# Optimization experiments

Hardware: AMD Instinct MI355X
Metric: run time of the kernel (lower is better)

Reference implementation:

```python
import jax, jax.numpy as jnp
import numpy as np

N, E, B, PG = 20000, 320000, 20, 1000  # nodes, edges, graphs, nodes-per-graph
H, L, NB, EI = 256, 6, 16, 8           # hidden, layers, node_base_dim, edge_in_dim
LN_EPS = 1e-5


def setup_inputs() -> dict:
    key = jax.random.key(0)
    ks = jax.random.split(key, 32)
    w = lambda i, s: (jax.random.normal(ks[i], s, jnp.float32) * 0.05)
    inp = {
        "x": jax.random.normal(ks[0], (N, NB), jnp.float32),
        "edge_attr": jax.random.normal(ks[1], (E, EI), jnp.float32),
        "c": jax.random.normal(ks[2], (B, PG), jnp.float32),
        "edge_index": jax.random.randint(ks[3], (2, E), 0, N),
        "node_gid": jnp.arange(N) // PG,   # batch.batch
        "node_lid": jnp.arange(N) % PG,    # node local index
        # edge_mlp: Linear(EI,H), ReLU, Linear(H,H)
        "ew1": w(4, (EI, H)), "eb1": jnp.zeros((H,), jnp.float32),
        "ew2": w(5, (H, H)),  "eb2": jnp.zeros((H,), jnp.float32),
        # input_proj: Linear(NB+1, H), SiLU
        "in_w": w(6, (NB + 1, H)), "in_b": jnp.zeros((H,), jnp.float32),
        # per-layer GINEConv edge lin (edge_dim -> in_channels)
        "lin_w": w(7, (L, H, H)), "lin_b": jnp.zeros((L, H), jnp.float32),
        # per-layer conv MLP: Linear(H,H), SiLU, Linear(H,H)
        "cw1": w(8, (L, H, H)), "cb1": jnp.zeros((L, H), jnp.float32),
        "cw2": w(9, (L, H, H)), "cb2": jnp.zeros((L, H), jnp.float32),
        # per-layer LayerNorm
        "ln_g": jnp.ones((L, H), jnp.float32), "ln_b": jnp.zeros((L, H), jnp.float32),
        # pool_attn: Linear(H,H), Tanh, Linear(H,1)
        "pa_w1": w(10, (H, H)), "pa_b1": jnp.zeros((H,), jnp.float32),
        "pa_w2": w(11, (H, 1)), "pa_b2": jnp.zeros((1,), jnp.float32),
        # head: Linear(H,H), SiLU, Linear(H,1)
        "hw1": w(12, (H, H)), "hb1": jnp.zeros((H,), jnp.float32),
        "hw2": w(13, (H, 1)), "hb2": jnp.zeros((1,), jnp.float32),
    }
    return inp


def _layer_norm(z, g, b):
    m = jnp.mean(z, axis=-1, keepdims=True)
    v = jnp.mean(jnp.square(z - m), axis=-1, keepdims=True)
    return (z - m) * jax.lax.rsqrt(v + LN_EPS) * g + b


def reference(x, edge_attr, c, edge_index, node_gid, node_lid,
              ew1, eb1, ew2, eb2, in_w, in_b,
              lin_w, lin_b, cw1, cb1, cw2, cb2, ln_g, ln_b,
              pa_w1, pa_b1, pa_w2, pa_b2, hw1, hb1, hw2, hb2):
    silu = jax.nn.silu
    # c_scalar: per-node coefficient
    c_scalar = c[node_gid, node_lid][:, None]                       # [N,1]
    xin = jnp.concatenate([x, c_scalar], axis=-1)                   # [N,NB+1]
    e = jax.nn.relu(edge_attr @ ew1 + eb1) @ ew2 + eb2              # [E,H]
    h = silu(xin @ in_w + in_b)                                     # [N,H]
    src, dst = edge_index[0], edge_index[1]
    for l in range(L):
        msg = jax.nn.relu(h[src] + (e @ lin_w[l] + lin_b[l]))       # [E,H]
        agg = jnp.zeros_like(h).at[dst].add(msg)                    # scatter-add
        z = h + agg                                                 # (1+eps)*x_i + agg, eps=0
        h_new = silu(z @ cw1[l] + cb1[l]) @ cw2[l] + cb2[l]
        h_new = _layer_norm(h_new, ln_g[l], ln_b[l])
        h = h + silu(h_new)
    # attention pooling: global softmax over nodes, renormalized per graph
    scores = jnp.tanh(h @ pa_w1 + pa_b1) @ pa_w2 + pa_b2            # [N,1]
    attn = jax.nn.softmax(scores, axis=0)                           # [N,1]
    seg_sum = jax.ops.segment_sum(attn[:, 0], node_gid, num_segments=B)  # [B]
    attn_n = attn[:, 0] / (seg_sum[node_gid] + 1e-8)                # [N]
    pooled = jax.ops.segment_sum(h * attn_n[:, None], node_gid, num_segments=B)  # [B,H]
    q = (silu(pooled @ hw1 + hb1) @ hw2 + hb2)[:, 0]                # [B]
    return q
```

## Files before the change

### kernel.cpp

```cpp
#include <hip/hip_runtime.h>
#include <hip/hip_bf16.h>
#include <cstdint>


#define NN 20000
#define EE 320000
#define BBG 20
#define PGN 1000
#define HH 256
#define LL 6

typedef short bf16x8 __attribute__((ext_vector_type(8)));
typedef float f32x4 __attribute__((ext_vector_type(4)));

__device__ __forceinline__ void async16(const void* g, void* l) {
  __builtin_amdgcn_global_load_lds(
      (const __attribute__((address_space(1))) unsigned int*)(uintptr_t)g,
      (__attribute__((address_space(3))) unsigned int*)(uintptr_t)l, 16, 0, 0);
}

__device__ __forceinline__ float siluf(float x) { return x / (1.f + __expf(-x)); }

__device__ __forceinline__ unsigned int f2bu(float x) {
  __hip_bfloat16 h = __float2bfloat16(x);
  return (unsigned int)*(unsigned short*)&h;
}

__device__ __forceinline__ float b2f(unsigned short u) {
  unsigned int v = ((unsigned int)u) << 16;
  return *(float*)&v;
}

enum { EPI_SILU = 1, EPI_PLAIN = 2, EPI_TANH = 3 };

template <int EPI>
__global__ void __launch_bounds__(256, 2) gemm256(
    const __hip_bfloat16* __restrict__ A, const __hip_bfloat16* __restrict__ Wt,
    const float* __restrict__ bias, int M, float* __restrict__ outf,
    __hip_bfloat16* __restrict__ outb) {
  __shared__ __align__(16) __hip_bfloat16 sA[128 * 32];
  __shared__ __align__(16) __hip_bfloat16 sB[128 * 32];

  const int t = threadIdx.x;
  const int wave = t >> 6, lane = t & 63;
  const int row0 = blockIdx.x * 128;
  const int col0 = blockIdx.y * 128;

  const int wrow = (wave >> 1) * 64;
  const int wcol = (wave & 1) * 64;
  const int fr = lane & 15, q = lane >> 4;

  f32x4 zero = {0.f, 0.f, 0.f, 0.f};
  f32x4 acc[4][4];
#pragma unroll
  for (int i = 0; i < 4; i++)
#pragma unroll
    for (int j = 0; j < 4; j++) acc[i][j] = zero;

  const int c1 = t, c2 = t + 256;
  const int lr1 = c1 >> 2, lr2 = c2 >> 2;
  const int q1 = (c1 & 3) ^ ((lr1 >> 1) & 3);
  const int q2 = (c2 & 3) ^ ((lr2 >> 1) & 3);
  int rA1 = row0 + lr1; if (rA1 >= M) rA1 = M - 1;
  int rA2 = row0 + lr2; if (rA2 >= M) rA2 = M - 1;
  const int rB1 = col0 + lr1, rB2 = col0 + lr2;

  for (int k0 = 0; k0 < 256; k0 += 32) {
    async16((const char*)(A + (size_t)rA1 * HH + k0) + q1 * 16,
            (char*)sA + wave * 1024);
    async16((const char*)(A + (size_t)rA2 * HH + k0) + q2 * 16,
            (char*)sA + 4096 + wave * 1024);
    async16((const char*)(Wt + (size_t)rB1 * HH + k0) + q1 * 16,
            (char*)sB + wave * 1024);
    async16((const char*)(Wt + (size_t)rB2 * HH + k0) + q2 * 16,
            (char*)sB + 4096 + wave * 1024);
    __syncthreads();
    bf16x8 af[4], bfr[4];
#pragma unroll
    for (int i = 0; i < 4; i++) {
      const int row = wrow + i * 16 + fr;
      af[i] = *(const bf16x8*)&sA[row * 32 + ((q ^ ((row >> 1) & 3))) * 8];
    }
#pragma unroll
    for (int j = 0; j < 4; j++) {
      const int row = wcol + j * 16 + fr;
      bfr[j] = *(const bf16x8*)&sB[row * 32 + ((q ^ ((row >> 1) & 3))) * 8];
    }
#pragma unroll
    for (int i = 0; i < 4; i++)
#pragma unroll
      for (int j = 0; j < 4; j++)
        acc[i][j] = __builtin_amdgcn_mfma_f32_16x16x32_bf16(af[i], bfr[j],
                                                            acc[i][j], 0, 0, 0);
    __syncthreads();
  }

#pragma unroll
  for (int j = 0; j < 4; j++) {
    const int col = col0 + wcol + j * 16 + fr;
    const float bs = bias[col];
#pragma unroll
    for (int i = 0; i < 4; i++) {
      const int lr0 = wrow + i * 16 + q * 4;
#pragma unroll
      for (int r = 0; r < 4; r++) {
        const int grow = row0 + lr0 + r;
        float v = acc[i][j][r] + bs;
        if (grow < M) {
          if (EPI == EPI_SILU) {
            outb[(size_t)grow * HH + col] = __float2bfloat16(siluf(v));
          } else if (EPI == EPI_PLAIN) {
            outf[(size_t)grow * HH + col] = v;
          } else {
            outb[(size_t)grow * HH + col] = __float2bfloat16(tanhf(v));
          }
        }
      }
    }
  }
}

__global__ void __launch_bounds__(256, 2) mlp_ln(
    const float* __restrict__ z, const __hip_bfloat16* __restrict__ W1t,
    const float* __restrict__ b1, const __hip_bfloat16* __restrict__ W2t,
    const float* __restrict__ b2, const float* __restrict__ g,
    const float* __restrict__ bbv, float* __restrict__ h,
    float* __restrict__ yzf, __hip_bfloat16* __restrict__ hb) {
  __shared__ __align__(16) char smem[20480 + 64 * 264 * 2];
  __hip_bfloat16* sA = (__hip_bfloat16*)smem;
  __hip_bfloat16* sB = (__hip_bfloat16*)(smem + 4096);
  unsigned short* sT = (unsigned short*)(smem + 20480);

  const int t = threadIdx.x;
  const int wave = t >> 6, lane = t & 63;
  const int row0 = blockIdx.x * 64;
  const int fr = lane & 15, q = lane >> 4;
  const int wr = wave * 16;

  const int lrA = t >> 2;
  const int qA = (t & 3) ^ ((lrA >> 1) & 3);
  int rA = row0 + lrA; if (rA >= NN) rA = NN - 1;
  int qB[4], rB[4];
#pragma unroll
  for (int p = 0; p < 4; p++) {
    const int c = t + p * 256;
    const int lr = c >> 2;
    qB[p] = (c & 3) ^ ((lr >> 1) & 3);
    rB[p] = lr;
  }

  f32x4 zero = {0.f, 0.f, 0.f, 0.f};
  f32x4 acc[16];
#pragma unroll
  for (int j = 0; j < 16; j++) acc[j] = zero;

  for (int k0 = 0; k0 < 256; k0 += 32) {
    {
      const float* s1 = z + (size_t)rA * HH + k0 + qA * 8;
      float4 a0 = *(const float4*)s1;
      float4 a1 = *(const float4*)(s1 + 4);
      uint4 u;
      u.x = f2bu(a0.x) | (f2bu(a0.y) << 16);
      u.y = f2bu(a0.z) | (f2bu(a0.w) << 16);
      u.z = f2bu(a1.x) | (f2bu(a1.y) << 16);
      u.w = f2bu(a1.z) | (f2bu(a1.w) << 16);
      *(uint4*)((char*)sA + t * 16) = u;
    }
#pragma unroll
    for (int p = 0; p < 4; p++)
      async16((const char*)(W1t + (size_t)rB[p] * HH + k0) + qB[p] * 16,
              (char*)sB + p * 4096 + wave * 1024);
    __syncthreads();
    bf16x8 af;
    {
      const int row = wr + fr;
      af = *(const bf16x8*)&sA[row * 32 + ((q ^ ((row >> 1) & 3))) * 8];
    }
#pragma unroll
    for (int j = 0; j < 16; j++) {
      const int row = j * 16 + fr;
      bf16x8 bfr = *(const bf16x8*)&sB[row * 32 + ((q ^ ((row >> 1) & 3))) * 8];
      acc[j] = __builtin_amdgcn_mfma_f32_16x16x32_bf16(af, bfr, acc[j], 0, 0, 0);
    }
    __syncthreads();
  }
#pragma unroll
  for (int j = 0; j < 16; j++) {
    const int col = j * 16 + fr;
    const float bs = b1[col];
    const int r0 = wr + q * 4;
#pragma unroll
    for (int r = 0; r < 4; r++)
      sT[(r0 + r) * 264 + col] =
          (unsigned short)f2bu(siluf(acc[j][r] + bs));
  }
#pragma unroll
  for (int j = 0; j < 16; j++) acc[j] = zero;

  for (int k0 = 0; k0 < 256; k0 += 32) {
#pragma unroll
    for (int p = 0; p < 4; p++)
      async16((const char*)(W2t + (size_t)rB[p] * HH + k0) + qB[p] * 16,
              (char*)sB + p * 4096 + wave * 1024);
    __syncthreads();
    bf16x8 af = *(const bf16x8*)&sT[(wr + fr) * 264 + k0 + q * 8];
#pragma unroll
    for (int j = 0; j < 16; j++) {
      const int row = j * 16 + fr;
      bf16x8 bfr = *(const bf16x8*)&sB[row * 32 + ((q ^ ((row >> 1) & 3))) * 8];
      acc[j] = __builtin_amdgcn_mfma_f32_16x16x32_bf16(af, bfr, acc[j], 0, 0, 0);
    }
    __syncthreads();
  }
#pragma unroll
  for (int j = 0; j < 16; j++) {
    const int col = j * 16 + fr;
    const float bs = b2[col];
    const int r0 = wr + q * 4;
#pragma unroll
    for (int r = 0; r < 4; r++)
      sT[(r0 + r) * 264 + col] = (unsigned short)f2bu(acc[j][r] + bs);
  }
  __syncthreads();

  for (int rr = 0; rr < 16; rr++) {
    const int r = wr + rr;
    const int grow = row0 + r;
    if (grow >= NN) break;
    float v[4];
    float s = 0.f;
#pragma unroll
    for (int i = 0; i < 4; i++) {
      v[i] = b2f(sT[r * 264 + lane + i * 64]);
      s += v[i];
    }
#pragma unroll
    for (int o = 32; o; o >>= 1) s += __shfl_xor(s, o);
    const float mean = s * (1.f / 256.f);
    float var = 0.f;
#pragma unroll
    for (int i = 0; i < 4; i++) { float d = v[i] - mean; var += d * d; }
#pragma unroll
    for (int o = 32; o; o >>= 1) var += __shfl_xor(var, o);
    const float rs = rsqrtf(var * (1.f / 256.f) + 1e-5f);
#pragma unroll
    for (int i = 0; i < 4; i++) {
      const int c = lane + i * 64;
      float ln = (v[i] - mean) * rs * g[c] + bbv[c];
      float si = siluf(ln);
      size_t idx = (size_t)grow * HH + c;
      float nh = h[idx] + si;
      h[idx] = nh;
      yzf[idx] = nh;
      hb[idx] = __float2bfloat16(nh);
    }
  }
}

__global__ void __launch_bounds__(256, 4) edge_fused(
    const __hip_bfloat16* __restrict__ te, const __hip_bfloat16* __restrict__ Wt,
    const float* __restrict__ bias, const __hip_bfloat16* __restrict__ hbv,
    const int* __restrict__ srcp, const int* __restrict__ dstp,
    float* __restrict__ z) {
  __shared__ __align__(16) char smem[32768];
  __shared__ int sSrc[128], sDst[128];
  __hip_bfloat16* sA = (__hip_bfloat16*)smem;
  __hip_bfloat16* sB = (__hip_bfloat16*)(smem + 16384);
  unsigned short* sRed = (unsigned short*)smem;

  const int t = threadIdx.x;
  const int wave = t >> 6, lane = t & 63;
  const int row0 = blockIdx.y * 128;
  const int col0 = blockIdx.x * 128;

  if (t < 128) { sSrc[t] = srcp[row0 + t]; sDst[t] = dstp[row0 + t]; }
  __syncthreads();

  const int wrow = (wave >> 1) * 64;
  const int fr = lane & 15, q = lane >> 4;
  const int rc = lane, rb = wave;

  f32x4 zero = {0.f, 0.f, 0.f, 0.f};
  f32x4 acc[4][4];
#pragma unroll
  for (int i = 0; i < 4; i++)
#pragma unroll
    for (int j = 0; j < 4; j++) acc[i][j] = zero;

  const int c1 = t, c2 = t + 256;
  const int lr1 = c1 >> 2, lr2 = c2 >> 2;
  const int q1 = (c1 & 3) ^ ((lr1 >> 1) & 3);
  const int q2 = (c2 & 3) ^ ((lr2 >> 1) & 3);
  const int rA1 = row0 + lr1, rA2 = row0 + lr2;
  const int rB1 = col0 + lr1, rB2 = col0 + lr2;

#pragma unroll
  for (int it = 0; it < 4; it++) {
    const int ka = it * 64, kb = ka + 32;
    async16((const char*)(te + (size_t)rA1 * HH + ka) + q1 * 16,
            (char*)sA + wave * 1024);
    async16((const char*)(te + (size_t)rA2 * HH + ka) + q2 * 16,
            (char*)sA + 4096 + wave * 1024);
    async16((const char*)(te + (size_t)rA1 * HH + kb) + q1 * 16,
            (char*)sA + 8192 + wave * 1024);
    async16((const char*)(te + (size_t)rA2 * HH + kb) + q2 * 16,
            (char*)sA + 12288 + wave * 1024);
    async16((const char*)(Wt + (size_t)rB1 * HH + ka) + q1 * 16,
            (char*)sB + wave * 1024);
    async16((const char*)(Wt + (size_t)rB2 * HH + ka) + q2 * 16,
            (char*)sB + 4096 + wave * 1024);
    async16((const char*)(Wt + (size_t)rB1 * HH + kb) + q1 * 16,
            (char*)sB + 8192 + wave * 1024);
    async16((const char*)(Wt + (size_t)rB2 * HH + kb) + q2 * 16,
            (char*)sB + 12288 + wave * 1024);
    __syncthreads();
#pragma unroll
    for (int half = 0; half < 2; half++) {
      const __hip_bfloat16* pA = sA + half * 4096;
      const __hip_bfloat16* pB = sB + half * 4096;
      bf16x8 af[4], bfr[4];
#pragma unroll
      for (int i = 0; i < 4; i++) {
        const int row = wrow + i * 16 + fr;
        af[i] = *(const bf16x8*)&pA[row * 32 + ((q ^ ((row >> 1) & 3))) * 8];
      }
#pragma unroll
      for (int j = 0; j < 4; j++) {
        const int row = (wave & 1) * 64 + j * 16 + fr;
        bfr[j] = *(const bf16x8*)&pB[row * 32 + ((q ^ ((row >> 1) & 3))) * 8];
      }
#pragma unroll
      for (int i = 0; i < 4; i++)
#pragma unroll
        for (int j = 0; j < 4; j++)
          acc[i][j] = __builtin_amdgcn_mfma_f32_16x16x32_bf16(af[i], bfr[j],
                                                              acc[i][j], 0, 0, 0);
    }
    __syncthreads();
  }

#pragma unroll
  for (int hf = 0; hf < 2; hf++) {
    if ((wave & 1) == hf) {
#pragma unroll
      for (int j = 0; j < 4; j++) {
        const int cl = j * 16 + fr;
        const float bs = bias[col0 + hf * 64 + cl];
#pragma unroll
        for (int i = 0; i < 4; i++) {
          const int r0 = wrow + i * 16 + q * 4;
          f32x4 v = acc[i][j];
          unsigned int p0 = f2bu(v[0] + bs) | (f2bu(v[1] + bs) << 16);
          unsigned int p1 = f2bu(v[2] + bs) | (f2bu(v[3] + bs) << 16);
          *(unsigned int*)&sRed[cl * 130 + r0] = p0;
          *(unsigned int*)&sRed[cl * 130 + r0 + 2] = p1;
        }
      }
    }
    __syncthreads();
    const int gcol = col0 + hf * 64 + rc;
    float a = 0.f;
    int cur = sDst[rb * 32];
    for (int ch = 0; ch < 4; ch++) {
      float hv8[8];
#pragma unroll
      for (int u = 0; u < 8; u++)
        hv8[u] = __bfloat162float(
            hbv[(size_t)sSrc[rb * 32 + ch * 8 + u] * HH + gcol]);
#pragma unroll
      for (int u = 0; u < 8; u++) {
        const int row = rb * 32 + ch * 8 + u;
        const int d = sDst[row];
        if (d != cur) {
          unsafeAtomicAdd(&z[(size_t)cur * HH + gcol], a);
          a = 0.f;
          cur = d;
        }
        float m = b2f(sRed[rc * 130 + row]) + hv8[u];
        a += m > 0.f ? m : 0.f;
      }
    }
    unsafeAtomicAdd(&z[(size_t)cur * HH + gcol], a);
    __syncthreads();
  }
}

__global__ void __launch_bounds__(256) hist_k(const int* __restrict__ edst,
                                              int* __restrict__ cnt) {
  const int e = blockIdx.x * 256 + threadIdx.x;
  if (e < EE) atomicAdd(&cnt[edst[e]], 1);
}

__global__ void __launch_bounds__(256) scan_k(const int* __restrict__ cnt,
                                              int* __restrict__ rowptr) {
  __shared__ int wsum[4];
  __shared__ int carry;
  const int t = threadIdx.x, wave = t >> 6, lane = t & 63;
  if (t == 0) carry = 0;
  __syncthreads();
  for (int base = 0; base < NN; base += 256) {
    const int idx = base + t;
    int v = (idx < NN) ? cnt[idx] : 0;
    int inc = v;
#pragma unroll
    for (int o = 1; o < 64; o <<= 1) {
      int u = __shfl_up(inc, o);
      if (lane >= o) inc += u;
    }
    if (lane == 63) wsum[wave] = inc;
    __syncthreads();
    int woff = 0;
    for (int w2 = 0; w2 < wave; w2++) woff += wsum[w2];
    if (idx < NN) rowptr[idx] = carry + woff + inc - v;
    const int total = wsum[0] + wsum[1] + wsum[2] + wsum[3];
    __syncthreads();
    if (t == 0) carry += total;
    __syncthreads();
  }
  if (t == 0) rowptr[NN] = carry;
}

__global__ void __launch_bounds__(256) scatter_k(
    const int* __restrict__ esrc, const int* __restrict__ edst,
    int* __restrict__ cursor, int* __restrict__ posof,
    int* __restrict__ srcp, int* __restrict__ dstp) {
  const int e = blockIdx.x * 256 + threadIdx.x;
  if (e < EE) {
    const int d = edst[e];
    const int pos = atomicAdd(&cursor[d], 1);
    posof[e] = pos;
    srcp[pos] = esrc[e];
    dstp[pos] = d;
  }
}

__global__ void __launch_bounds__(256) edge_hidden(
    const float* __restrict__ ea, const float* __restrict__ ew1,
    const float* __restrict__ eb1, const int* __restrict__ posof,
    __hip_bfloat16* __restrict__ tout) {
  __shared__ float w[8 * 256];
  __shared__ float b[256];
  __shared__ float sea[16 * 8];
  __shared__ int spos[16];
  const int t = threadIdx.x;
  for (int i = t; i < 8 * 256; i += 256) w[i] = ew1[i];
  b[t] = eb1[t];
  const int e0 = blockIdx.x * 16;
  if (t < 128) sea[t] = ea[(size_t)e0 * 8 + t];
  if (t < 16) spos[t] = posof[e0 + t];
  __syncthreads();
  for (int e = 0; e < 16; e++) {
    float a = b[t];
#pragma unroll
    for (int j = 0; j < 8; j++) a += sea[e * 8 + j] * w[j * 256 + t];
    tout[(size_t)spos[e] * HH + t] = __float2bfloat16(a > 0.f ? a : 0.f);
  }
}

__global__ void __launch_bounds__(256) fold_edge_w(
    const float* __restrict__ ew2, const float* __restrict__ lin_w,
    const float* __restrict__ eb2, const float* __restrict__ lin_b,
    __hip_bfloat16* __restrict__ Wlt, float* __restrict__ bl) {
  const int l = blockIdx.x >> 8, j = blockIdx.x & 255;
  const int c = threadIdx.x;
  __shared__ float row[256];
  row[c] = ew2[j * 256 + c];
  __syncthreads();
  const float* lw = lin_w + (size_t)l * 65536;
  float a = 0.f;
  for (int k = 0; k < 256; k++) a += row[k] * lw[k * 256 + c];
  Wlt[((size_t)l * 256 + c) * 256 + j] = __float2bfloat16(a);
  if (j == 0) {
    float s = lin_b[l * 256 + c];
    for (int k = 0; k < 256; k++) s += eb2[k] * lw[k * 256 + c];
    bl[l * 256 + c] = s;
  }
}

__global__ void __launch_bounds__(256) tcast_all(
    const float* __restrict__ cw1, const float* __restrict__ cw2,
    const float* __restrict__ paw1, __hip_bfloat16* __restrict__ cw1t,
    __hip_bfloat16* __restrict__ cw2t, __hip_bfloat16* __restrict__ paw1t) {
  const int b = blockIdx.x;
  const float* s;
  __hip_bfloat16* d;
  if (b < 1536) { int l = b >> 8; s = cw1 + (size_t)l * 65536; d = cw1t + (size_t)l * 65536; }
  else if (b < 3072) { int l = (b - 1536) >> 8; s = cw2 + (size_t)l * 65536; d = cw2t + (size_t)l * 65536; }
  else { s = paw1; d = paw1t; }
  const int r = b & 255, c = threadIdx.x;
  d[(size_t)c * 256 + r] = __float2bfloat16(s[(size_t)r * 256 + c]);
}

__global__ void __launch_bounds__(256) node_init(
    const float* __restrict__ x, const float* __restrict__ cc,
    const int* __restrict__ gid, const int* __restrict__ lid,
    const float* __restrict__ in_w, const float* __restrict__ in_b,
    float* __restrict__ h, float* __restrict__ yzf,
    __hip_bfloat16* __restrict__ hb) {
  __shared__ float w[17 * 256];
  __shared__ float b[256];
  __shared__ float sx[16 * 17];
  const int t = threadIdx.x;
  for (int i = t; i < 17 * 256; i += 256) w[i] = in_w[i];
  b[t] = in_b[t];
  const int n0 = blockIdx.x * 16;
  sx[(t >> 4) * 17 + (t & 15)] = x[(size_t)(n0 + (t >> 4)) * 16 + (t & 15)];
  if (t < 16) {
    int n = n0 + t;
    sx[t * 17 + 16] = cc[gid[n] * PGN + lid[n]];
  }
  __syncthreads();
  for (int e = 0; e < 16; e++) {
    float a = b[t];
#pragma unroll
    for (int j = 0; j < 17; j++) a += sx[e * 17 + j] * w[j * 256 + t];
    float s = siluf(a);
    size_t idx = (size_t)(n0 + e) * HH + t;
    h[idx] = s;
    yzf[idx] = s;
    hb[idx] = __float2bfloat16(s);
  }
}

__global__ void __launch_bounds__(256) score_k(
    const __hip_bfloat16* __restrict__ s1, const float* __restrict__ pw2,
    const float* __restrict__ pb2, float* __restrict__ scores,
    float* __restrict__ pmax) {
  __shared__ float w2[256];
  __shared__ float bm[4];
  const int t = threadIdx.x, wave = t >> 6, lane = t & 63;
  w2[t] = pw2[t];
  __syncthreads();
  const size_t row = (size_t)blockIdx.x * 4 + wave;
  float a = 0.f;
#pragma unroll
  for (int i = 0; i < 4; i++) {
    int c = lane + i * 64;
    a += __bfloat162float(s1[row * HH + c]) * w2[c];
  }
#pragma unroll
  for (int o = 32; o; o >>= 1) a += __shfl_xor(a, o);
  float sc = a + pb2[0];
  if (lane == 0) { scores[row] = sc; bm[wave] = sc; }
  __syncthreads();
  if (t == 0) pmax[blockIdx.x] = fmaxf(fmaxf(bm[0], bm[1]), fmaxf(bm[2], bm[3]));
}

__global__ void __launch_bounds__(256) gmax_k(const float* __restrict__ pmax,
                                              int n, float* __restrict__ gmax) {
  const int t = threadIdx.x;
  float m = -3.4e38f;
  for (int i = t; i < n; i += 256) m = fmaxf(m, pmax[i]);
#pragma unroll
  for (int o = 32; o; o >>= 1) m = fmaxf(m, __shfl_xor(m, o));
  __shared__ float wm[4];
  if ((t & 63) == 0) wm[t >> 6] = m;
  __syncthreads();
  if (t == 0) gmax[0] = fmaxf(fmaxf(wm[0], wm[1]), fmaxf(wm[2], wm[3]));
}

__global__ void __launch_bounds__(256) esum_k(
    const float* __restrict__ scores, const int* __restrict__ gid,
    const float* __restrict__ gmax, float* __restrict__ en,
    float* __restrict__ seg) {
  __shared__ float ls[BBG + 1];
  const int t = threadIdx.x;
  if (t < BBG + 1) ls[t] = 0.f;
  __syncthreads();
  const int n = blockIdx.x * 256 + t;
  if (n < NN) {
    float e = __expf(scores[n] - gmax[0]);
    en[n] = e;
    atomicAdd(&ls[gid[n]], e);
    atomicAdd(&ls[BBG], e);
  }
  __syncthreads();
  if (t < BBG + 1) unsafeAtomicAdd(&seg[t], ls[t]);
}

__global__ void __launch_bounds__(256) pooled_k(
    const float* __restrict__ h, const float* __restrict__ en,
    const float* __restrict__ seg, float* __restrict__ pooled) {
  const int g = blockIdx.x / 40, ch = blockIdx.x % 40;
  const int c = threadIdx.x;
  const int n0 = g * PGN + ch * 25;
  float a = 0.f;
  for (int i = 0; i < 25; i++) {
    int n = n0 + i;
    a += en[n] * h[(size_t)n * HH + c];
  }
  const float inv = 1.f / (seg[g] + 1e-8f * seg[BBG]);
  unsafeAtomicAdd(&pooled[g * HH + c], a * inv);
}

__global__ void __launch_bounds__(256) head_k(
    const float* __restrict__ pooled, const float* __restrict__ hw1,
    const float* __restrict__ hb1, const float* __restrict__ hw2,
    const float* __restrict__ hb2, float* __restrict__ qout) {
  const int b = blockIdx.x, c = threadIdx.x;
  __shared__ float p[256];
  __shared__ float wsum[4];
  p[c] = pooled[b * 256 + c];
  __syncthreads();
  float a = hb1[c];
  for (int k = 0; k < 256; k++) a += p[k] * hw1[k * 256 + c];
  float v = siluf(a) * hw2[c];
#pragma unroll
  for (int o = 32; o; o >>= 1) v += __shfl_xor(v, o);
  if ((c & 63) == 0) wsum[c >> 6] = v;
  __syncthreads();
  if (c == 0) qout[b] = wsum[0] + wsum[1] + wsum[2] + wsum[3] + hb2[0];
}

extern "C" void kernel_launch(void* const* d_in, const int* in_sizes, int n_in,
                              void* d_out, int out_size, void* d_ws, size_t ws_size,
                              hipStream_t stream) {
  const float* x = (const float*)d_in[0];
  const float* edge_attr = (const float*)d_in[1];
  const float* cc = (const float*)d_in[2];
  const int* edge_index = (const int*)d_in[3];
  const int* node_gid = (const int*)d_in[4];
  const int* node_lid = (const int*)d_in[5];
  const float* ew1 = (const float*)d_in[6];
  const float* eb1 = (const float*)d_in[7];
  const float* ew2 = (const float*)d_in[8];
  const float* eb2 = (const float*)d_in[9];
  const float* in_w = (const float*)d_in[10];
  const float* in_b = (const float*)d_in[11];
  const float* lin_w = (const float*)d_in[12];
  const float* lin_b = (const float*)d_in[13];
  const float* cw1 = (const float*)d_in[14];
  const float* cb1 = (const float*)d_in[15];
  const float* cw2 = (const float*)d_in[16];
  const float* cb2 = (const float*)d_in[17];
  const float* ln_g = (const float*)d_in[18];
  const float* ln_b = (const float*)d_in[19];
  const float* pa_w1 = (const float*)d_in[20];
  const float* pa_b1 = (const float*)d_in[21];
  const float* pa_w2 = (const float*)d_in[22];
  const float* pa_b2 = (const float*)d_in[23];
  const float* hw1 = (const float*)d_in[24];
  const float* hb1 = (const float*)d_in[25];
  const float* hw2 = (const float*)d_in[26];
  const float* hb2 = (const float*)d_in[27];
  float* qout = (float*)d_out;

  char* w = (char*)d_ws;
  auto alloc = [&](size_t bytes) {
    char* p = w;
    w += (bytes + 255) & ~(size_t)255;
    return p;
  };
  __hip_bfloat16* t_e = (__hip_bfloat16*)alloc((size_t)EE * HH * 2);
  float* h = (float*)alloc((size_t)NN * HH * 4);
  float* yzf = (float*)alloc((size_t)NN * HH * 4);
  __hip_bfloat16* hb = (__hip_bfloat16*)alloc((size_t)NN * HH * 2);
  __hip_bfloat16* t2 = (__hip_bfloat16*)alloc((size_t)NN * HH * 2);
  __hip_bfloat16* Wlt = (__hip_bfloat16*)alloc((size_t)LL * HH * HH * 2);
  float* bl = (float*)alloc((size_t)LL * HH * 4);
  __hip_bfloat16* cw1t = (__hip_bfloat16*)alloc((size_t)LL * HH * HH * 2);
  __hip_bfloat16* cw2t = (__hip_bfloat16*)alloc((size_t)LL * HH * HH * 2);
  __hip_bfloat16* paw1t = (__hip_bfloat16*)alloc((size_t)HH * HH * 2);
  float* scores = (float*)alloc((size_t)NN * 4);
  float* pmax = (float*)alloc(5008 * 4);
  float* en = (float*)alloc((size_t)NN * 4);
  float* seg = (float*)alloc((BBG + 1) * 4);
  float* gmax = (float*)alloc(4);
  float* pooled = (float*)alloc((size_t)BBG * HH * 4);
  int* cnt = (int*)alloc((size_t)NN * 4);
  int* rowptr = (int*)alloc((size_t)(NN + 1) * 4);
  int* cursor = (int*)alloc((size_t)NN * 4);
  int* posof = (int*)alloc((size_t)EE * 4);
  int* srcp = (int*)alloc((size_t)EE * 4);
  int* dstp = (int*)alloc((size_t)EE * 4);

  const int* esrc = edge_index;
  const int* edst = edge_index + EE;

  hipMemsetAsync(cnt, 0, (size_t)NN * 4, stream);
  hipMemsetAsync(seg, 0, (BBG + 1) * 4, stream);
  hipMemsetAsync(pooled, 0, (size_t)BBG * HH * 4, stream);

  hist_k<<<(EE + 255) / 256, 256, 0, stream>>>(edst, cnt);
  scan_k<<<1, 256, 0, stream>>>(cnt, rowptr);
  hipMemcpyAsync(cursor, rowptr, (size_t)NN * 4, hipMemcpyDeviceToDevice, stream);
  scatter_k<<<(EE + 255) / 256, 256, 0, stream>>>(esrc, edst, cursor, posof,
                                                  srcp, dstp);

  fold_edge_w<<<LL * 256, 256, 0, stream>>>(ew2, lin_w, eb2, lin_b, Wlt, bl);
  tcast_all<<<3328, 256, 0, stream>>>(cw1, cw2, pa_w1, cw1t, cw2t, paw1t);
  edge_hidden<<<EE / 16, 256, 0, stream>>>(edge_attr, ew1, eb1, posof, t_e);
  node_init<<<NN / 16, 256, 0, stream>>>(x, cc, node_gid, node_lid, in_w, in_b,
                                         h, yzf, hb);

  dim3 gE(2, EE / 128), gN((NN + 127) / 128, 2);
  const int gMLP = (NN + 63) / 64;
  for (int l = 0; l < LL; l++) {
    edge_fused<<<gE, 256, 0, stream>>>(t_e, Wlt + (size_t)l * HH * HH,
                                       bl + l * HH, hb, srcp, dstp, yzf);
    mlp_ln<<<gMLP, 256, 0, stream>>>(
        yzf, cw1t + (size_t)l * HH * HH, cb1 + l * HH,
        cw2t + (size_t)l * HH * HH, cb2 + l * HH, ln_g + l * HH, ln_b + l * HH,
        h, yzf, hb);
  }

  gemm256<EPI_TANH><<<gN, 256, 0, stream>>>(hb, paw1t, pa_b1, NN, nullptr, t2);
  score_k<<<NN / 4, 256, 0, stream>>>(t2, pa_w2, pa_b2, scores, pmax);
  gmax_k<<<1, 256, 0, stream>>>(pmax, NN / 4, gmax);
  esum_k<<<(NN + 255) / 256, 256, 0, stream>>>(scores, node_gid, gmax, en, seg);
  pooled_k<<<BBG * 40, 256, 0, stream>>>(h, en, seg, pooled);
  head_k<<<BBG, 256, 0, stream>>>(pooled, hw1, hb1, hw2, hb2, qout);
}
```

Before: 1.207 ms.

## Halve mlp_ln row tile to 32 and split output columns across wave pairs

The fused MLP+LayerNorm kernel now handles 32 rows per block instead of 64. The four waves form a 2x2 grid of row tiles and 128-column halves, so each wave holds 8 accumulators instead of 16. Shared memory shrinks, launch bounds rise to 4 blocks per CU, and the grid doubles, all aimed at more occupancy and better CU fill. The cost is that every weight tile is loaded from global memory twice as often per row, and only half the threads load the A tile. The row bounds checks are removed on the basis that NN divides evenly by 32.

After: 1.113 ms. 1.08x faster.

```diff
diff --git a/kernel.cpp b/kernel.cpp
--- a/kernel.cpp
+++ b/kernel.cpp
@@ -120,26 +120,26 @@
   }
 }
 
-__global__ void __launch_bounds__(256, 2) mlp_ln(
+__global__ void __launch_bounds__(256, 4) mlp_ln(
     const float* __restrict__ z, const __hip_bfloat16* __restrict__ W1t,
     const float* __restrict__ b1, const __hip_bfloat16* __restrict__ W2t,
     const float* __restrict__ b2, const float* __restrict__ g,
     const float* __restrict__ bbv, float* __restrict__ h,
     float* __restrict__ yzf, __hip_bfloat16* __restrict__ hb) {
-  __shared__ __align__(16) char smem[20480 + 64 * 264 * 2];
+  __shared__ __align__(16) char smem[2048 + 16384 + 32 * 264 * 2];
   __hip_bfloat16* sA = (__hip_bfloat16*)smem;
-  __hip_bfloat16* sB = (__hip_bfloat16*)(smem + 4096);
-  unsigned short* sT = (unsigned short*)(smem + 20480);
+  __hip_bfloat16* sB = (__hip_bfloat16*)(smem + 2048);
+  unsigned short* sT = (unsigned short*)(smem + 18432);
 
   const int t = threadIdx.x;
   const int wave = t >> 6, lane = t & 63;
-  const int row0 = blockIdx.x * 64;
+  const int row0 = blockIdx.x * 32;
   const int fr = lane & 15, q = lane >> 4;
-  const int wr = wave * 16;
+  const int rt = wave & 1;
+  const int chf = wave >> 1;
 
   const int lrA = t >> 2;
   const int qA = (t & 3) ^ ((lrA >> 1) & 3);
-  int rA = row0 + lrA; if (rA >= NN) rA = NN - 1;
   int qB[4], rB[4];
 #pragma unroll
   for (int p = 0; p < 4; p++) {
@@ -150,13 +150,16 @@
   }
 
   f32x4 zero = {0.f, 0.f, 0.f, 0.f};
-  f32x4 acc[16];
-#pragma unroll
-  for (int j = 0; j < 16; j++) acc[j] = zero;
+  f32x4 acc[8];
+#pragma unroll
+  for (int j = 0; j < 8; j++) acc[j] = zero;
+
+  const int arow = rt * 16 + fr;
+  const int aswz = (q ^ ((arow >> 1) & 3)) * 8;
 
   for (int k0 = 0; k0 < 256; k0 += 32) {
-    {
-      const float* s1 = z + (size_t)rA * HH + k0 + qA * 8;
+    if (t < 128) {
+      const float* s1 = z + (size_t)(row0 + lrA) * HH + k0 + qA * 8;
       float4 a0 = *(const float4*)s1;
       float4 a1 = *(const float4*)(s1 + 4);
       uint4 u;
@@ -171,31 +174,26 @@
       async16((const char*)(W1t + (size_t)rB[p] * HH + k0) + qB[p] * 16,
               (char*)sB + p * 4096 + wave * 1024);
     __syncthreads();
-    bf16x8 af;
-    {
-      const int row = wr + fr;
-      af = *(const bf16x8*)&sA[row * 32 + ((q ^ ((row >> 1) & 3))) * 8];
-    }
-#pragma unroll
-    for (int j = 0; j < 16; j++) {
-      const int row = j * 16 + fr;
+    bf16x8 af = *(const bf16x8*)&sA[arow * 32 + aswz];
+#pragma unroll
+    for (int j = 0; j < 8; j++) {
+      const int row = chf * 128 + j * 16 + fr;
       bf16x8 bfr = *(const bf16x8*)&sB[row * 32 + ((q ^ ((row >> 1) & 3))) * 8];
       acc[j] = __builtin_amdgcn_mfma_f32_16x16x32_bf16(af, bfr, acc[j], 0, 0, 0);
     }
     __syncthreads();
   }
 #pragma unroll
-  for (int j = 0; j < 16; j++) {
-    const int col = j * 16 + fr;
+  for (int j = 0; j < 8; j++) {
+    const int col = chf * 128 + j * 16 + fr;
     const float bs = b1[col];
-    const int r0 = wr + q * 4;
+    const int r0 = rt * 16 + q * 4;
 #pragma unroll
     for (int r = 0; r < 4; r++)
-      sT[(r0 + r) * 264 + col] =
-          (unsigned short)f2bu(siluf(acc[j][r] + bs));
-  }
-#pragma unroll
-  for (int j = 0; j < 16; j++) acc[j] = zero;
+      sT[(r0 + r) * 264 + col] = (unsigned short)f2bu(siluf(acc[j][r] + bs));
+  }
+#pragma unroll
+  for (int j = 0; j < 8; j++) acc[j] = zero;
 
   for (int k0 = 0; k0 < 256; k0 += 32) {
 #pragma unroll
@@ -203,30 +201,29 @@
       async16((const char*)(W2t + (size_t)rB[p] * HH + k0) + qB[p] * 16,
               (char*)sB + p * 4096 + wave * 1024);
     __syncthreads();
-    bf16x8 af = *(const bf16x8*)&sT[(wr + fr) * 264 + k0 + q * 8];
-#pragma unroll
-    for (int j = 0; j < 16; j++) {
-      const int row = j * 16 + fr;
+    bf16x8 af = *(const bf16x8*)&sT[arow * 264 + k0 + q * 8];
+#pragma unroll
+    for (int j = 0; j < 8; j++) {
+      const int row = chf * 128 + j * 16 + fr;
       bf16x8 bfr = *(const bf16x8*)&sB[row * 32 + ((q ^ ((row >> 1) & 3))) * 8];
       acc[j] = __builtin_amdgcn_mfma_f32_16x16x32_bf16(af, bfr, acc[j], 0, 0, 0);
     }
     __syncthreads();
   }
 #pragma unroll
-  for (int j = 0; j < 16; j++) {
-    const int col = j * 16 + fr;
+  for (int j = 0; j < 8; j++) {
+    const int col = chf * 128 + j * 16 + fr;
     const float bs = b2[col];
-    const int r0 = wr + q * 4;
+    const int r0 = rt * 16 + q * 4;
 #pragma unroll
     for (int r = 0; r < 4; r++)
       sT[(r0 + r) * 264 + col] = (unsigned short)f2bu(acc[j][r] + bs);
   }
   __syncthreads();
 
-  for (int rr = 0; rr < 16; rr++) {
-    const int r = wr + rr;
+  for (int rr = 0; rr < 8; rr++) {
+    const int r = wave * 8 + rr;
     const int grow = row0 + r;
-    if (grow >= NN) break;
     float v[4];
     float s = 0.f;
 #pragma unroll
@@ -694,7 +691,7 @@
                                          h, yzf, hb);
 
   dim3 gE(2, EE / 128), gN((NN + 127) / 128, 2);
-  const int gMLP = (NN + 63) / 64;
+  const int gMLP = NN / 32;
   for (int l = 0; l < LL; l++) {
     edge_fused<<<gE, 256, 0, stream>>>(t_e, Wlt + (size_t)l * HH * HH,
                                        bl + l * HH, hb, srcp, dstp, yzf);
```
